# Optimization experiments

Hardware: AMD Instinct MI355X
Metric: run time of the kernel (lower is better)

Reference implementation:

```python
import jax, jax.numpy as jnp
import numpy as np
from jax import lax

EPS = 1e-5  # BatchNorm eps; eval-mode BN with running_mean=0, running_var=1


def _bn(v, g, b):
    return v * (g / jnp.sqrt(1.0 + EPS)) + b


def setup_inputs() -> dict:
    key = jax.random.key(0)
    ks = jax.random.split(key, 8)
    B, I, O, H, W, E, K, r = 16, 128, 128, 128, 128, 16, 3, 8
    Ir, Or = I // r, O // r
    f = jax.random.normal
    return {
        "x": f(ks[0], (B, I, H, W), jnp.float32),
        "experts": f(ks[1], (E, O, I, K, K), jnp.float32) * 0.05,
        "rw1": f(ks[2], (Ir, I), jnp.float32) * 0.05,
        "rbn1_g": jnp.ones((Ir,), jnp.float32),
        "rbn1_b": jnp.zeros((Ir,), jnp.float32),
        "rw2": f(ks[3], (I, Ir), jnp.float32) * 0.05,
        "rbn2_g": jnp.ones((I,), jnp.float32),
        "rbn2_b": jnp.zeros((I,), jnp.float32),
        "rw3": f(ks[4], (E, I), jnp.float32) * 0.05,
        "rb3": jnp.zeros((E,), jnp.float32),
        "ca_w1": f(ks[5], (Or, O), jnp.float32) * 0.05,
        "ca_bn1_g": jnp.ones((Or,), jnp.float32),
        "ca_bn1_b": jnp.zeros((Or,), jnp.float32),
        "ca_w2": f(ks[6], (O, Or), jnp.float32) * 0.05,
        "ca_bn2_g": jnp.ones((O,), jnp.float32),
        "ca_bn2_b": jnp.zeros((O,), jnp.float32),
        "sa_w": f(ks[7], (1, 2, 7, 7), jnp.float32) * 0.05,
        "sa_bn_g": jnp.ones((1,), jnp.float32),
        "sa_bn_b": jnp.zeros((1,), jnp.float32),
    }


def reference(x, experts, rw1, rbn1_g, rbn1_b, rw2, rbn2_g, rbn2_b, rw3, rb3,
              ca_w1, ca_bn1_g, ca_bn1_b, ca_w2, ca_bn2_g, ca_bn2_b,
              sa_w, sa_bn_g, sa_bn_b):
    B, I, H, W = x.shape
    E, O, _, K, _ = experts.shape
    # --- routing: avgpool -> 1x1 conv (matmul) -> BN -> ReLU -> 1x1 -> BN -> sigmoid -> 1x1 -> softmax
    p = jnp.mean(x, axis=(2, 3))                                  # [B, I]
    h = jax.nn.relu(_bn(p @ rw1.T, rbn1_g, rbn1_b))               # [B, I/r]
    g = jax.nn.sigmoid(_bn(h @ rw2.T, rbn2_g, rbn2_b))            # [B, I]
    rweights = jax.nn.softmax(g @ rw3.T + rb3, axis=1)            # [B, E]
    # --- expert-weighted kernel generation as a single GEMM
    w = jnp.einsum('be,eoihw->boihw', rweights, experts)          # [B, O, I, K, K]
    # --- per-sample conv via grouped conv (groups = B), stride=1, padding=1
    out = lax.conv_general_dilated(
        x.reshape(1, B * I, H, W),
        w.reshape(B * O, I, K, K),
        window_strides=(1, 1), padding=((1, 1), (1, 1)),
        dimension_numbers=('NCHW', 'OIHW', 'NCHW'),
        feature_group_count=B,
    ).reshape(B, O, H, W)
    # --- SE channel attention
    cp = jnp.mean(out, axis=(2, 3))                               # [B, O]
    ch = jax.nn.relu(_bn(cp @ ca_w1.T, ca_bn1_g, ca_bn1_b))
    cw = jax.nn.sigmoid(_bn(ch @ ca_w2.T, ca_bn2_g, ca_bn2_b))    # [B, O]
    out = out * cw[:, :, None, None]
    # --- CBAM spatial attention
    sp = jnp.concatenate([jnp.mean(out, axis=1, keepdims=True),
                          jnp.max(out, axis=1, keepdims=True)], axis=1)  # [B,2,H,W]
    sw = lax.conv_general_dilated(sp, sa_w, (1, 1), ((3, 3), (3, 3)),
                                  dimension_numbers=('NCHW', 'OIHW', 'NCHW'))
    sw = jax.nn.sigmoid(_bn(sw, sa_bn_g.reshape(1, 1, 1, 1), sa_bn_b.reshape(1, 1, 1, 1)))
    out = out * sw
    # --- residual (in_channels == out_channels -> Identity)
    return out + x
```

## Files before the change

### kernel.cpp

```cpp
#include <hip/hip_runtime.h>

typedef unsigned short ushort_t;
typedef __attribute__((ext_vector_type(4))) float float4_t;
typedef __attribute__((ext_vector_type(8))) short short8_t;
typedef __attribute__((ext_vector_type(8))) unsigned short ushort8_t;
typedef __attribute__((ext_vector_type(4))) unsigned short ushort4_t;

__device__ __forceinline__ ushort_t f2bf(float f) {
    unsigned u = __builtin_bit_cast(unsigned, f);
    u = (u + 0x7fffu + ((u >> 16) & 1u)) >> 16;
    return (ushort_t)u;
}
__device__ __forceinline__ ushort_t f2h(float f) {
    return __builtin_bit_cast(unsigned short, (_Float16)f);
}
__device__ __forceinline__ float h2f(ushort_t u) {
    return (float)__builtin_bit_cast(_Float16, u);
}

__device__ __forceinline__ void gld16(const void* g, void* l) {
    __builtin_amdgcn_global_load_lds(
        (const __attribute__((address_space(1))) unsigned int*)g,
        (__attribute__((address_space(3))) unsigned int*)l, 16, 0, 0);
}


__global__ __launch_bounds__(256) void init_kernel(float* __restrict__ p, float* __restrict__ st,
                                                   float* __restrict__ sp, ushort_t* __restrict__ xn) {
    int t = blockIdx.x * 256 + threadIdx.x;
    if (t < 2048) { p[t] = 0.f; return; }
    if (t < 18432) { st[t - 2048] = 0.f; return; }
    if (t < 18432 + 574592) { sp[t - 18432] = 0.f; return; }
    int e = t - (18432 + 574592);
    if (e < 1056768) {
        int b = e / 66048;
        int r = e % 66048;
        int pix = r >> 7, i = r & 127;
        int hp, wp;
        if (pix < 130)      { hp = 0;   wp = pix; }
        else if (pix < 260) { hp = 129; wp = pix - 130; }
        else { int q = pix - 260; hp = 1 + (q >> 1); wp = (q & 1) ? 129 : 0; }
        xn[((b * 130 + hp) * 130 + wp) * 128 + i] = 0;
    }
}

__global__ __launch_bounds__(256) void transpose_kernel(const float* __restrict__ x,
                                                        ushort_t* __restrict__ xn,
                                                        float* __restrict__ p,
                                                        float* __restrict__ st) {
    __shared__ float tile[128][65];
    int blk = blockIdx.x;
    int wt = blk & 1, h = (blk >> 1) & 127, b = blk >> 8;
    int w0 = wt * 64;
    int tid = threadIdx.x;
    int wl = tid & 63, ig = tid >> 6;
    const float* src = x + ((long)(b * 128) * 128 + h) * 128 + w0 + wl;
    #pragma unroll
    for (int i = ig; i < 128; i += 4) tile[i][wl] = src[(long)i * 16384];
    __syncthreads();
    if (tid < 128) {
        float s = 0.f;
        #pragma unroll
        for (int w = 0; w < 64; ++w) s += tile[tid][w];
        atomicAdd(&p[b * 128 + tid], s * (1.0f / 16384.0f));
        float* sb = st + ((b << 7) + tid) * 8;
        if (h == 0)   atomicAdd(&sb[0], s);
        if (h == 127) atomicAdd(&sb[1], s);
        float edge = tile[tid][wt ? 63 : 0];
        atomicAdd(&sb[wt ? 3 : 2], edge);
        if (h == 0)   sb[wt ? 5 : 4] = edge;
        if (h == 127) sb[wt ? 7 : 6] = edge;
    }
    int l16 = tid & 15, wq = tid >> 4;
    #pragma unroll
    for (int pass = 0; pass < 4; ++pass) {
        int w = wq + pass * 16;
        ushort8_t v;
        #pragma unroll
        for (int j = 0; j < 8; ++j) v[j] = f2bf(tile[l16 * 8 + j][w]);
        *(ushort8_t*)&xn[((b * 130 + h + 1) * 130 + (w0 + w + 1)) * 128 + l16 * 8] = v;
    }
}

__global__ __launch_bounds__(256) void wgen_kernel(const float* __restrict__ experts,
        const float* __restrict__ p, const float* __restrict__ st,
        const float* __restrict__ rw1, const float* __restrict__ g1, const float* __restrict__ b1,
        const float* __restrict__ rw2, const float* __restrict__ g2, const float* __restrict__ b2,
        const float* __restrict__ rw3, const float* __restrict__ rb3,
        ushort_t* __restrict__ w2, float* __restrict__ cp) {
    int o = blockIdx.x;
    int tid = threadIdx.x;
    int lane = tid & 63, wave = tid >> 6;
    __shared__ __align__(16) float ex[16 * 1152];
    __shared__ float sg[16][128];
    __shared__ float sh[16][16];
    __shared__ float sl[16][16];
    __shared__ float rwl[16][16];
    __shared__ float cpw[4][8];

    const float* ebase = experts + (long)o * 1152;
    #pragma unroll
    for (int j = 0; j < 4; ++j) {
        int e = wave * 4 + j;
        const char* src = (const char*)(ebase + (long)e * 147456) + lane * 16;
        char* dst = (char*)&ex[e * 1152];
        #pragma unroll
        for (int k = 0; k < 5; ++k) {
            if (k < 4 || lane < 32)
                gld16(src + k * 1024, dst + k * 1024);
        }
    }

    const float bns = rsqrtf(1.0f + 1e-5f);
    {   int b = tid >> 4, j = tid & 15;
        float s = 0.f;
        for (int i = 0; i < 128; ++i) s += p[b * 128 + i] * rw1[j * 128 + i];
        s = s * (g1[j] * bns) + b1[j];
        sh[b][j] = fmaxf(s, 0.f); }
    __syncthreads();
    for (int c = 0; c < 8; ++c) {
        int idx = tid + c * 256;
        int b = idx >> 7, j = idx & 127;
        float s = 0.f;
        for (int k = 0; k < 16; ++k) s += sh[b][k] * rw2[j * 16 + k];
        s = s * (g2[j] * bns) + b2[j];
        sg[b][j] = 1.0f / (1.0f + expf(-s));
    }
    __syncthreads();
    {   int b = tid >> 4, e = tid & 15;
        float s = rb3[e];
        for (int j = 0; j < 128; ++j) s += sg[b][j] * rw3[e * 128 + j];
        sl[b][e] = s; }
    __syncthreads();
    {   int b = tid >> 4, e = tid & 15;
        float m = -1e30f;
        for (int k = 0; k < 16; ++k) m = fmaxf(m, sl[b][k]);
        float num = expf(sl[b][e] - m), den = 0.f;
        for (int k = 0; k < 16; ++k) den += expf(sl[b][k] - m);
        rwl[b][e] = num / den; }
    asm volatile("s_waitcnt vmcnt(0)" ::: "memory");
    __syncthreads();

    int i = tid & 127, half = tid >> 7;
    float acc[8][9];
    #pragma unroll
    for (int b = 0; b < 8; ++b)
        #pragma unroll
        for (int d = 0; d < 9; ++d) acc[b][d] = 0.f;
    for (int e = 0; e < 16; ++e) {
        float v[9];
        #pragma unroll
        for (int d = 0; d < 9; ++d) v[d] = ex[e * 1152 + i * 9 + d];
        #pragma unroll
        for (int b = 0; b < 8; ++b) {
            float r = rwl[half * 8 + b][e];
            #pragma unroll
            for (int d = 0; d < 9; ++d) acc[b][d] += v[d] * r;
        }
    }
    float cps[8];
    #pragma unroll
    for (int bb2 = 0; bb2 < 8; ++bb2) {
        int b = half * 8 + bb2;
        const float* sb = st + ((b << 7) + i) * 8;
        float T = p[(b << 7) + i] * 16384.f;
        float r0 = sb[0], r127 = sb[1], c0 = sb[2], c127 = sb[3];
        float x00 = sb[4], x0127 = sb[5], x1270 = sb[6], x127127 = sb[7];
        float S0 = T - r127 - c127 + x127127;
        float S1 = T - r127;
        float S2 = T - r127 - c0 + x1270;
        float S3 = T - c127;
        float S4 = T;
        float S5 = T - c0;
        float S6 = T - r0 - c127 + x0127;
        float S7 = T - r0;
        float S8 = T - r0 - c0 + x00;
        cps[bb2] = acc[bb2][0] * S0 + acc[bb2][1] * S1 + acc[bb2][2] * S2 +
                   acc[bb2][3] * S3 + acc[bb2][4] * S4 + acc[bb2][5] * S5 +
                   acc[bb2][6] * S6 + acc[bb2][7] * S7 + acc[bb2][8] * S8;
    }
    #pragma unroll
    for (int bb2 = 0; bb2 < 8; ++bb2)
        for (int msk = 1; msk < 64; msk <<= 1) cps[bb2] += __shfl_xor(cps[bb2], msk, 64);
    if (lane == 0) {
        #pragma unroll
        for (int bb2 = 0; bb2 < 8; ++bb2) cpw[wave][bb2] = cps[bb2];
    }
    #pragma unroll
    for (int b = 0; b < 8; ++b)
        #pragma unroll
        for (int d = 0; d < 9; ++d)
            w2[(((half * 8 + b) * 9 + d) << 14) + (o << 7) + i] = f2bf(acc[b][d]);
    __syncthreads();
    if (tid < 16) {
        int hf = tid >> 3, idx = tid & 7;
        cp[(tid << 7) + o] = cpw[hf * 2][idx] + cpw[hf * 2 + 1][idx];
    }
}

__global__ __launch_bounds__(256) void se_kernel(const float* __restrict__ cp,
        const float* __restrict__ w1, const float* __restrict__ g1, const float* __restrict__ b1,
        const float* __restrict__ w2, const float* __restrict__ g2, const float* __restrict__ b2,
        float* __restrict__ cw) {
    __shared__ float sc[16][128];
    __shared__ float sh[16][16];
    int tid = threadIdx.x;
    const float bns = rsqrtf(1.0f + 1e-5f);
    for (int c = 0; c < 8; ++c) {
        int idx = tid + c * 256;
        sc[idx >> 7][idx & 127] = cp[idx] * (1.0f / 16384.0f);
    }
    __syncthreads();
    {   int b = tid >> 4, j = tid & 15;
        float s = 0.f;
        for (int o = 0; o < 128; ++o) s += sc[b][o] * w1[j * 128 + o];
        s = s * (g1[j] * bns) + b1[j];
        sh[b][j] = fmaxf(s, 0.f); }
    __syncthreads();
    for (int c = 0; c < 8; ++c) {
        int idx = tid + c * 256;
        int b = idx >> 7, o = idx & 127;
        float s = 0.f;
        for (int k = 0; k < 16; ++k) s += sh[b][k] * w2[o * 16 + k];
        s = s * (g2[o] * bns) + b2[o];
        cw[idx] = 1.0f / (1.0f + expf(-s));
    }
}

struct __align__(16) ConvSmem {
    union {
        struct { ushort_t X[16640]; ushort_t A[4][4096]; } t;
        float c[4224];
    };
};

__global__ __launch_bounds__(256, 2) void conv_kernel(const ushort_t* __restrict__ xn,
                                                      const ushort_t* __restrict__ w2,
                                                      const float* __restrict__ cw,
                                                      ushort_t* __restrict__ outi,
                                                      float* __restrict__ sp) {
    __shared__ ConvSmem sm;
    __shared__ float scw[128];
    __shared__ float cmb[2][128];
    int bh = (blockIdx.x & 7) * 256 + (blockIdx.x >> 3);
    int b = bh >> 7, h = bh & 127;
    int tid = threadIdx.x;
    int lane = tid & 63, wave = tid >> 6;
    int wm = wave & 1, wn = wave >> 1;
    int q = lane >> 4, nl = lane & 15;

    float4_t acc[4][4];
    #pragma unroll
    for (int mi = 0; mi < 4; ++mi)
        #pragma unroll
        for (int ni = 0; ni < 4; ++ni) acc[mi][ni] = (float4_t){0.f, 0.f, 0.f, 0.f};

    const ushort_t* xbase = xn + (b * 130 + h) * 16640;
    const ushort_t* abase = w2 + (long)b * 147456;

    float cwv = 0.f;
    if (tid < 128) cwv = cw[(b << 7) + tid];

    auto stageX = [&](int dy) {
        const ushort_t* xrow = xbase + dy * 16640;
        #pragma unroll
        for (int seg = wave; seg < 33; seg += 4) {
            if (seg < 32 || lane < 32) {
                int lofs = seg * 512 + lane * 8;
                int pp = lofs >> 7;
                int jb = (lofs & 127) >> 3;
                gld16(xrow + (pp << 7) + ((jb ^ (pp & 15)) << 3), &sm.t.X[seg * 512]);
            }
        }
    };
    auto stageA = [&](int c) {
        int dy = c / 12, rem = c % 12, dx = rem >> 2, ic = rem & 3;
        const ushort_t* ab = abase + (dy * 3 + dx) * 16384 + ic * 32;
        int buf = c & 3;
        int ol = lane >> 2;
        int jsrc = (lane & 3) ^ ((ol >> 1) & 3);
        #pragma unroll
        for (int inst = 0; inst < 2; ++inst) {
            int ob = wave * 32 + inst * 16;
            gld16(ab + (ob + ol) * 128 + (jsrc << 3), &sm.t.A[buf][ob * 32]);
        }
    };

    short8_t afr[2][4], bfr[2][4];
    auto readFrag = [&](int cc) {
        int pb = cc & 1;
        int dx = (cc % 12) >> 2, ic = cc & 3;
        const ushort_t* ap = &sm.t.A[cc & 3][0];
        #pragma unroll
        for (int mi = 0; mi < 4; ++mi) {
            int o = wm * 64 + mi * 16 + nl;
            afr[pb][mi] = *(const short8_t*)&ap[(o << 5) + ((q ^ ((o >> 1) & 3)) << 3)];
        }
        #pragma unroll
        for (int ni = 0; ni < 4; ++ni) {
            int pp = wn * 64 + ni * 16 + nl + dx;
            int J = ic * 4 + q;
            bfr[pb][ni] = *(const short8_t*)&sm.t.X[(pp << 7) + ((J ^ (pp & 15)) << 3)];
        }
    };
    auto domfma = [&](int pb) {
        __builtin_amdgcn_s_setprio(1);
        #pragma unroll
        for (int mi = 0; mi < 4; ++mi)
            #pragma unroll
            for (int ni = 0; ni < 4; ++ni)
                acc[mi][ni] = __builtin_amdgcn_mfma_f32_16x16x32_bf16(
                    afr[pb][mi], bfr[pb][ni], acc[mi][ni], 0, 0, 0);
        __builtin_amdgcn_s_setprio(0);
    };

    stageX(0);
    stageA(0); stageA(1); stageA(2);
    if (tid < 128) scw[tid] = cwv;
    asm volatile("s_waitcnt vmcnt(0)" ::: "memory");
    __builtin_amdgcn_s_barrier();
    readFrag(0);

    #pragma unroll
    for (int c = 0; c < 36; ++c) {
        if (c + 3 < 36) stageA(c + 3);
        const bool bnd = (c == 11 || c == 23);
        if (!bnd && c + 1 < 36) readFrag(c + 1);
        domfma(c & 1);
        if (bnd) {
            __builtin_amdgcn_s_barrier();
            stageX(c == 11 ? 1 : 2);
            asm volatile("s_waitcnt vmcnt(0)" ::: "memory");
            __builtin_amdgcn_s_barrier();
            readFrag(c + 1);
        } else if (c < 35) {
            if (c == 33)
                asm volatile("s_waitcnt vmcnt(0)" ::: "memory");
            else if (!(c == 0 || c == 12 || c == 24 || c == 34))
                asm volatile("s_waitcnt vmcnt(2)" ::: "memory");
            __builtin_amdgcn_s_barrier();
        }
    }

    ushort_t* outb = outi + (((long)(b << 7)) << 14) + (h << 7);
    int wpx = tid & 127, g = tid >> 7;
    float wsum = 0.f, wmax = -1e30f;
    #pragma unroll
    for (int os = 0; os < 4; ++os) {
        __syncthreads();
        if (wm == (os >> 1)) {
            #pragma unroll
            for (int mi2 = 0; mi2 < 2; ++mi2) {
                int mi = (os & 1) * 2 + mi2;
                #pragma unroll
                for (int ni = 0; ni < 4; ++ni) {
                    float4_t v = acc[mi][ni];
                    int orow = mi2 * 16 + q * 4;
                    int w = wn * 64 + ni * 16 + nl;
                    #pragma unroll
                    for (int rr = 0; rr < 4; ++rr) sm.c[(orow + rr) * 132 + w] = v[rr];
                }
            }
        }
        __syncthreads();
        int row = tid >> 4, j = tid & 15;
        #pragma unroll
        for (int pass = 0; pass < 2; ++pass) {
            int r2 = pass * 16 + row;
            ushort8_t v;
            #pragma unroll
            for (int k = 0; k < 8; ++k) v[k] = f2h(sm.c[r2 * 132 + j * 8 + k]);
            *(ushort8_t*)&outb[((long)(os * 32 + r2) << 14) + j * 8] = v;
        }
        #pragma unroll
        for (int r = 0; r < 16; ++r) {
            int orow = g * 16 + r;
            float v = sm.c[orow * 132 + wpx] * scw[os * 32 + orow];
            wsum += v;
            wmax = fmaxf(wmax, v);
        }
    }
    if (g == 1) { cmb[0][wpx] = wsum; cmb[1][wpx] = wmax; }
    __syncthreads();
    if (g == 0) {
        wsum += cmb[0][wpx];
        wmax = fmaxf(wmax, cmb[1][wpx]);
        float* d = sp + b * 2 * 17956;
        d[(h + 3) * 134 + (wpx + 3)] = wsum * (1.0f / 128.0f);
        d[17956 + (h + 3) * 134 + (wpx + 3)] = wmax;
    }
}

__global__ __launch_bounds__(256) void sattn_kernel(const float* __restrict__ sp,
        const float* __restrict__ k98, const float* __restrict__ g, const float* __restrict__ bb,
        const float* __restrict__ cw, const float* __restrict__ x,
        const ushort_t* __restrict__ outi, float* __restrict__ out) {
    int b = blockIdx.x >> 7, h = blockIdx.x & 127;
    int tid = threadIdx.x;
    __shared__ float ls[2][7][134];
    __shared__ float lk[98];
    __shared__ float sws[128];
    __shared__ float scw[128];
    const float* sb = sp + b * 2 * 17956;
    for (int idx = tid; idx < 2 * 7 * 134; idx += 256) {
        int c = idx / 938, rr = idx % 938;
        int ky = rr / 134, wp = rr % 134;
        ls[c][ky][wp] = sb[c * 17956 + (h + ky) * 134 + wp];
    }
    if (tid < 98) lk[tid] = k98[tid];
    if (tid >= 128) scw[tid - 128] = cw[(b << 7) + (tid - 128)];
    __syncthreads();
    if (tid < 128) {
        float s = 0.f;
        #pragma unroll
        for (int c = 0; c < 2; ++c)
            #pragma unroll
            for (int ky = 0; ky < 7; ++ky)
                #pragma unroll
                for (int kx = 0; kx < 7; ++kx)
                    s += ls[c][ky][tid + kx] * lk[c * 49 + ky * 7 + kx];
        s = s * (g[0] * rsqrtf(1.0f + 1e-5f)) + bb[0];
        sws[tid] = 1.0f / (1.0f + expf(-s));
    }
    __syncthreads();
    int w4 = tid & 31, og = tid >> 5;
    long base = (((long)b << 21) + (h << 7)) + (w4 << 2);
    float4_t sv = *(const float4_t*)&sws[w4 << 2];
    #pragma unroll
    for (int o = og; o < 128; o += 8) {
        long idx = base + ((long)o << 14);
        ushort4_t hv = *(const ushort4_t*)&outi[idx];
        float4_t ov = (float4_t){h2f(hv[0]), h2f(hv[1]), h2f(hv[2]), h2f(hv[3])};
        float4_t xv = *(const float4_t*)&x[idx];
        float4_t r = ov * scw[o] * sv + xv;
        *(float4_t*)&out[idx] = r;
    }
}

extern "C" void kernel_launch(void* const* d_in, const int* in_sizes, int n_in,
                              void* d_out, int out_size, void* d_ws, size_t ws_size,
                              hipStream_t stream) {
    const float* x       = (const float*)d_in[0];
    const float* experts = (const float*)d_in[1];
    const float* rw1     = (const float*)d_in[2];
    const float* rbn1_g  = (const float*)d_in[3];
    const float* rbn1_b  = (const float*)d_in[4];
    const float* rw2     = (const float*)d_in[5];
    const float* rbn2_g  = (const float*)d_in[6];
    const float* rbn2_b  = (const float*)d_in[7];
    const float* rw3     = (const float*)d_in[8];
    const float* rb3     = (const float*)d_in[9];
    const float* ca_w1   = (const float*)d_in[10];
    const float* ca_bn1g = (const float*)d_in[11];
    const float* ca_bn1b = (const float*)d_in[12];
    const float* ca_w2   = (const float*)d_in[13];
    const float* ca_bn2g = (const float*)d_in[14];
    const float* ca_bn2b = (const float*)d_in[15];
    const float* sa_w    = (const float*)d_in[16];
    const float* sa_g    = (const float*)d_in[17];
    const float* sa_b    = (const float*)d_in[18];
    float* out = (float*)d_out;
    char* ws = (char*)d_ws;

    ushort_t* xn   = (ushort_t*)(ws);
    ushort_t* w2   = (ushort_t*)(ws + 69222400);
    float*    p    = (float*)(ws + 73940992);
    float*    cp   = (float*)(ws + 73949184);
    float*    cw   = (float*)(ws + 73958400);
    float*    sp   = (float*)(ws + 73966592);
    ushort_t* outi = (ushort_t*)(ws + 76264960);
    float*    st   = (float*)(ws + 143373824);

    hipLaunchKernelGGL(init_kernel, dim3(6445), dim3(256), 0, stream, p, st, sp, xn);
    hipLaunchKernelGGL(transpose_kernel, dim3(4096), dim3(256), 0, stream, x, xn, p, st);
    hipLaunchKernelGGL(wgen_kernel, dim3(128), dim3(256), 0, stream,
                       experts, p, st, rw1, rbn1_g, rbn1_b, rw2, rbn2_g, rbn2_b, rw3, rb3,
                       w2, cp);
    hipLaunchKernelGGL(se_kernel, dim3(1), dim3(256), 0, stream,
                       cp, ca_w1, ca_bn1g, ca_bn1b, ca_w2, ca_bn2g, ca_bn2b, cw);
    hipLaunchKernelGGL(conv_kernel, dim3(2048), dim3(256), 0, stream, xn, w2, cw, outi, sp);
    hipLaunchKernelGGL(sattn_kernel, dim3(2048), dim3(256), 0, stream,
                       sp, sa_w, sa_g, sa_b, cw, x, outi, out);
}
```

Before: 469.0 us.

## Fuse SE kernel into wgen via last-block counter and move border stats to init

The single-block SE kernel is folded into wgen_kernel: each block publishes its channel sums, bumps a global counter, and the last block to finish runs the SE MLP and writes cw. This drops one kernel launch and its serialization gap. The per-sample border sums and corners that the transpose kernel gathered with many atomics are now computed directly by extra blocks in init_kernel, which reads x border rows and columns. The counter relies on threadfence ordering, and the last block does serial tail work.

```diff
diff --git a/kernel.cpp b/kernel.cpp
--- a/kernel.cpp
+++ b/kernel.cpp
@@ -25,16 +25,45 @@
 }
 
 
-__global__ __launch_bounds__(256) void init_kernel(float* __restrict__ p, float* __restrict__ st,
-                                                   float* __restrict__ sp, ushort_t* __restrict__ xn) {
-    int t = blockIdx.x * 256 + threadIdx.x;
-    if (t < 2048) { p[t] = 0.f; return; }
-    if (t < 18432) { st[t - 2048] = 0.f; return; }
-    if (t < 18432 + 574592) { sp[t - 18432] = 0.f; return; }
-    int e = t - (18432 + 574592);
-    if (e < 1056768) {
-        int b = e / 66048;
-        int r = e % 66048;
+__global__ __launch_bounds__(256) void init_kernel(float* __restrict__ p,
+                                                   float* __restrict__ sp,
+                                                   ushort_t* __restrict__ xn,
+                                                   float* __restrict__ st,
+                                                   unsigned* __restrict__ wcnt,
+                                                   const float* __restrict__ x) {
+    int blk = blockIdx.x;
+    int tid = threadIdx.x;
+    if (blk >= 6381) {
+        int bi = blk - 6381;
+        const float* xb = x + (long)bi * 16384;
+        int half = tid >> 7, t = tid & 127;
+        __shared__ float red[2][2][128];
+        __shared__ float corn[4];
+        float rv = half ? xb[16256 + t] : xb[t];
+        float cv = half ? xb[t * 128 + 127] : xb[t * 128];
+        red[0][half][t] = rv;
+        red[1][half][t] = cv;
+        if (tid == 0)   corn[0] = rv;
+        if (tid == 127) corn[1] = rv;
+        if (tid == 128) corn[2] = rv;
+        if (tid == 255) corn[3] = rv;
+        __syncthreads();
+        int wave = tid >> 6, lane = tid & 63;
+        int kind = wave >> 1, hf = wave & 1;
+        float s = red[kind][hf][lane] + red[kind][hf][lane + 64];
+        for (int msk = 1; msk < 64; msk <<= 1) s += __shfl_xor(s, msk, 64);
+        if (lane == 0) st[bi * 8 + kind * 2 + hf] = s;
+        if (tid < 4) st[bi * 8 + 4 + tid] = corn[tid];
+        return;
+    }
+    int t = blk * 256 + tid;
+    if (t < 2048) { p[t] = 0.f; if (t == 0) *wcnt = 0u; return; }
+    t -= 2048;
+    if (t < 574592) { sp[t] = 0.f; return; }
+    t -= 574592;
+    if (t < 1056768) {
+        int b = t / 66048;
+        int r = t % 66048;
         int pix = r >> 7, i = r & 127;
         int hp, wp;
         if (pix < 130)      { hp = 0;   wp = pix; }
@@ -46,8 +75,7 @@
 
 __global__ __launch_bounds__(256) void transpose_kernel(const float* __restrict__ x,
                                                         ushort_t* __restrict__ xn,
-                                                        float* __restrict__ p,
-                                                        float* __restrict__ st) {
+                                                        float* __restrict__ p) {
     __shared__ float tile[128][65];
     int blk = blockIdx.x;
     int wt = blk & 1, h = (blk >> 1) & 127, b = blk >> 8;
@@ -63,13 +91,6 @@
         #pragma unroll
         for (int w = 0; w < 64; ++w) s += tile[tid][w];
         atomicAdd(&p[b * 128 + tid], s * (1.0f / 16384.0f));
-        float* sb = st + ((b << 7) + tid) * 8;
-        if (h == 0)   atomicAdd(&sb[0], s);
-        if (h == 127) atomicAdd(&sb[1], s);
-        float edge = tile[tid][wt ? 63 : 0];
-        atomicAdd(&sb[wt ? 3 : 2], edge);
-        if (h == 0)   sb[wt ? 5 : 4] = edge;
-        if (h == 127) sb[wt ? 7 : 6] = edge;
     }
     int l16 = tid & 15, wq = tid >> 4;
     #pragma unroll
@@ -87,7 +108,10 @@
         const float* __restrict__ rw1, const float* __restrict__ g1, const float* __restrict__ b1,
         const float* __restrict__ rw2, const float* __restrict__ g2, const float* __restrict__ b2,
         const float* __restrict__ rw3, const float* __restrict__ rb3,
-        ushort_t* __restrict__ w2, float* __restrict__ cp) {
+        const float* __restrict__ cw1, const float* __restrict__ cg1, const float* __restrict__ cb1,
+        const float* __restrict__ cw2, const float* __restrict__ cg2, const float* __restrict__ cb2,
+        ushort_t* __restrict__ w2, float* __restrict__ cp, float* __restrict__ cw,
+        unsigned* __restrict__ wcnt) {
     int o = blockIdx.x;
     int tid = threadIdx.x;
     int lane = tid & 63, wave = tid >> 6;
@@ -97,6 +121,7 @@
     __shared__ float sl[16][16];
     __shared__ float rwl[16][16];
     __shared__ float cpw[4][8];
+    __shared__ int lastf;
 
     const float* ebase = experts + (long)o * 1152;
     #pragma unroll
@@ -194,35 +219,36 @@
     __syncthreads();
     if (tid < 16) {
         int hf = tid >> 3, idx = tid & 7;
-        cp[(tid << 7) + o] = cpw[hf * 2][idx] + cpw[hf * 2 + 1][idx];
-    }
-}
-
-__global__ __launch_bounds__(256) void se_kernel(const float* __restrict__ cp,
-        const float* __restrict__ w1, const float* __restrict__ g1, const float* __restrict__ b1,
-        const float* __restrict__ w2, const float* __restrict__ g2, const float* __restrict__ b2,
-        float* __restrict__ cw) {
-    __shared__ float sc[16][128];
-    __shared__ float sh[16][16];
-    int tid = threadIdx.x;
-    const float bns = rsqrtf(1.0f + 1e-5f);
+        float v = cpw[hf * 2][idx] + cpw[hf * 2 + 1][idx];
+        __hip_atomic_store(&cp[(tid << 7) + o], v, __ATOMIC_RELAXED,
+                           __HIP_MEMORY_SCOPE_AGENT);
+    }
+
+    __threadfence();
+    __syncthreads();
+    if (tid == 0) lastf = (atomicAdd(wcnt, 1u) == 127u) ? 1 : 0;
+    __syncthreads();
+    if (!lastf) return;
+    __threadfence();
     for (int c = 0; c < 8; ++c) {
         int idx = tid + c * 256;
-        sc[idx >> 7][idx & 127] = cp[idx] * (1.0f / 16384.0f);
+        float v = __hip_atomic_load(&cp[idx], __ATOMIC_RELAXED, __HIP_MEMORY_SCOPE_AGENT);
+        sg[idx >> 7][idx & 127] = v * (1.0f / 16384.0f);
     }
     __syncthreads();
     {   int b = tid >> 4, j = tid & 15;
         float s = 0.f;
-        for (int o = 0; o < 128; ++o) s += sc[b][o] * w1[j * 128 + o];
-        s = s * (g1[j] * bns) + b1[j];
+        for (int oo = 0; oo < 128; ++oo) s += sg[b][oo] * cw1[j * 128 + oo];
+        s = s * (cg1[j] * bns) + cb1[j];
         sh[b][j] = fmaxf(s, 0.f); }
     __syncthreads();
     for (int c = 0; c < 8; ++c) {
         int idx = tid + c * 256;
-        int b = idx >> 7, o = idx & 127;
+        int b = idx >> 7, oo = idx & 127;
         float s = 0.f;
-        for (int k = 0; k < 16; ++k) s += sh[b][k] * w2[o * 16 + k];
-        s = s * (g2[o] * bns) + b2[o];
+        #pragma unroll
+        for (int k = 0; k < 16; ++k) s += sh[b][k] * cw2[oo * 16 + k];
+        s = s * (cg2[oo] * bns) + cb2[oo];
         cw[idx] = 1.0f / (1.0f + expf(-s));
     }
 }
@@ -466,18 +492,19 @@
     ushort_t* w2   = (ushort_t*)(ws + 69222400);
     float*    p    = (float*)(ws + 73940992);
     float*    cp   = (float*)(ws + 73949184);
+    unsigned* wcnt = (unsigned*)(ws + 73957376);
     float*    cw   = (float*)(ws + 73958400);
     float*    sp   = (float*)(ws + 73966592);
     ushort_t* outi = (ushort_t*)(ws + 76264960);
     float*    st   = (float*)(ws + 143373824);
 
-    hipLaunchKernelGGL(init_kernel, dim3(6445), dim3(256), 0, stream, p, st, sp, xn);
-    hipLaunchKernelGGL(transpose_kernel, dim3(4096), dim3(256), 0, stream, x, xn, p, st);
+    hipLaunchKernelGGL(init_kernel, dim3(8429), dim3(256), 0, stream,
+                       p, sp, xn, st, wcnt, x);
+    hipLaunchKernelGGL(transpose_kernel, dim3(4096), dim3(256), 0, stream, x, xn, p);
     hipLaunchKernelGGL(wgen_kernel, dim3(128), dim3(256), 0, stream,
                        experts, p, st, rw1, rbn1_g, rbn1_b, rw2, rbn2_g, rbn2_b, rw3, rb3,
-                       w2, cp);
-    hipLaunchKernelGGL(se_kernel, dim3(1), dim3(256), 0, stream,
-                       cp, ca_w1, ca_bn1g, ca_bn1b, ca_w2, ca_bn2g, ca_bn2b, cw);
+                       ca_w1, ca_bn1g, ca_bn1b, ca_w2, ca_bn2g, ca_bn2b,
+                       w2, cp, cw, wcnt);
     hipLaunchKernelGGL(conv_kernel, dim3(2048), dim3(256), 0, stream, xn, w2, cw, outi, sp);
     hipLaunchKernelGGL(sattn_kernel, dim3(2048), dim3(256), 0, stream,
                        sp, sa_w, sa_g, sa_b, cw, x, outi, out);
```

Result: slower. 481.0 us (+2.6%).
